# Kernel tuning notes

Hardware: AMD Instinct MI355X
Metric: run time of the kernel (lower is better)

The kernel has to match this reference:

```python
import jax, jax.numpy as jnp
import numpy as np


def setup_inputs() -> dict:
    key = jax.random.key(0)
    kq, kk, kv = jax.random.split(key, 3)
    B, H, S, D = 2, 16, 2048, 64
    query = jax.random.normal(kq, (B, H, S, D), dtype=jnp.float32)
    k = jax.random.normal(kk, (B, H, S, D), dtype=jnp.float32)
    value = jax.random.normal(kv, (B, H, S, D), dtype=jnp.float32)
    attn_mask = jnp.zeros((B, H, S, S), dtype=jnp.float32)
    return {"query": query, "key": k, "value": value, "attn_mask": attn_mask}


def reference(query, key, value, attn_mask):
    # scores: [B, H, Lq, Lk]
    dk = jnp.asarray(query.shape[-1], query.dtype)
    scores = jnp.einsum("bhqd,bhkd->bhqk", query, key) / jnp.sqrt(dk)
    scores = scores + attn_mask
    attention = jax.nn.softmax(scores, axis=-1)
    # dropout is identity at inference (training=False)
    context = jnp.einsum("bhqk,bhkd->bhqd", attention, value)
    return (context, attention)
```

## Files before the change

kernel.cpp:

```cpp
#include <hip/hip_runtime.h>
#include <stdint.h>


#if defined(__has_builtin)
#if __has_builtin(__builtin_amdgcn_exp2f)
#define EXP2(x) __builtin_amdgcn_exp2f(x)
#else
#define EXP2(x) exp2f(x)
#endif
#else
#define EXP2(x) exp2f(x)
#endif

typedef _Float16 half8 __attribute__((ext_vector_type(8)));
typedef _Float16 half2v __attribute__((ext_vector_type(2)));
typedef float f32x4 __attribute__((ext_vector_type(4)));

static constexpr int S = 2048;
static constexpr int D = 64;
static constexpr int BH = 32;
static constexpr int QT = 16;
static constexpr float LOG2E = 1.4426950408889634f;
static constexpr float SCL2E = 0.125f * LOG2E;

__device__ __forceinline__ half8 cvt8(float4 a, float4 b) {
  half8 r;
  r[0] = (_Float16)a.x; r[1] = (_Float16)a.y; r[2] = (_Float16)a.z; r[3] = (_Float16)a.w;
  r[4] = (_Float16)b.x; r[5] = (_Float16)b.y; r[6] = (_Float16)b.z; r[7] = (_Float16)b.w;
  return r;
}

__device__ __forceinline__ unsigned pack2(float a, float b) {
  half2v h; h[0] = (_Float16)a; h[1] = (_Float16)b;
  return __builtin_bit_cast(unsigned, h);
}

__device__ __forceinline__ float2 unpack2(unsigned u) {
  half2v h = __builtin_bit_cast(half2v, u);
  return make_float2((float)h[0], (float)h[1]);
}

__global__ __launch_bounds__(256, 3)
void sdpa_kernel(const float* __restrict__ Qg, const float* __restrict__ Kg,
                 const float* __restrict__ Vg, const float* __restrict__ Mg,
                 float* __restrict__ Cg, float* __restrict__ Ag) {
  const int bh = blockIdx.x & (BH - 1);
  const int qt = blockIdx.x >> 5;

  const int tid  = threadIdx.x;
  const int w    = tid >> 6;
  const int lane = tid & 63;
  const int quad = lane >> 4;
  const int l16  = lane & 15;

  const int q0 = qt * QT;
  const float* Qb = Qg + (size_t)bh * S * D;
  const float* Kb = Kg + (size_t)bh * S * D;
  const float* Vb = Vg + (size_t)bh * S * D;
  const float* Mb = Mg + (size_t)bh * S * S;
  float* Ab = Ag + (size_t)bh * S * S;
  float* Cb = Cg + (size_t)bh * S * D;

  __shared__ float partial[4][16];
  __shared__ float invsum[16];
  __shared__ _Float16 pbuf[4][16 * 72];
  __shared__ float ctxbuf[4][16 * 68];

  half8 a0, a1;
  {
    const float* qp = Qb + (size_t)(q0 + l16) * D + quad * 8;
    float4 x0 = *(const float4*)(qp);
    float4 x1 = *(const float4*)(qp + 4);
    float4 x2 = *(const float4*)(qp + 32);
    float4 x3 = *(const float4*)(qp + 36);
    a0 = cvt8(x0, x1);
    a1 = cvt8(x2, x3);
  }

  const int c0 = w * 512;
  float rs0 = 0.f, rs1 = 0.f, rs2 = 0.f, rs3 = 0.f;
  uint2 strip[32];

#pragma unroll
  for (int t = 0; t < 32; ++t) {
    const int col = c0 + t * 16;
    const int n   = col + l16;
    const float* kp = Kb + (size_t)n * D + quad * 8;
    float4 k0 = *(const float4*)(kp);
    float4 k1 = *(const float4*)(kp + 4);
    float4 k2 = *(const float4*)(kp + 32);
    float4 k3 = *(const float4*)(kp + 36);
    const float* mp = Mb + (size_t)(q0 + quad * 4) * S + n;
    float m0 = mp[0];
    float m1 = mp[S];
    float m2 = mp[2 * S];
    float m3 = mp[3 * S];

    half8 b0 = cvt8(k0, k1);
    half8 b1 = cvt8(k2, k3);
    f32x4 acc = {0.f, 0.f, 0.f, 0.f};
    acc = __builtin_amdgcn_mfma_f32_16x16x32_f16(a0, b0, acc, 0, 0, 0);
    acc = __builtin_amdgcn_mfma_f32_16x16x32_f16(a1, b1, acc, 0, 0, 0);

    float p0 = EXP2(fmaf(acc[0], SCL2E, m0 * LOG2E));
    float p1 = EXP2(fmaf(acc[1], SCL2E, m1 * LOG2E));
    float p2 = EXP2(fmaf(acc[2], SCL2E, m2 * LOG2E));
    float p3 = EXP2(fmaf(acc[3], SCL2E, m3 * LOG2E));
    rs0 += p0; rs1 += p1; rs2 += p2; rs3 += p3;
    strip[t].x = pack2(p0, p1);
    strip[t].y = pack2(p2, p3);
  }

#pragma unroll
  for (int off = 8; off >= 1; off >>= 1) {
    rs0 += __shfl_xor(rs0, off, 64);
    rs1 += __shfl_xor(rs1, off, 64);
    rs2 += __shfl_xor(rs2, off, 64);
    rs3 += __shfl_xor(rs3, off, 64);
  }
  if (l16 == 0) {
    partial[w][quad * 4 + 0] = rs0;
    partial[w][quad * 4 + 1] = rs1;
    partial[w][quad * 4 + 2] = rs2;
    partial[w][quad * 4 + 3] = rs3;
  }
  __syncthreads();
  if (tid < 16) {
    float s = partial[0][tid] + partial[1][tid] + partial[2][tid] + partial[3][tid];
    invsum[tid] = 1.0f / s;
  }
  __syncthreads();
  const float inv0 = invsum[quad * 4 + 0];
  const float inv1 = invsum[quad * 4 + 1];
  const float inv2 = invsum[quad * 4 + 2];
  const float inv3 = invsum[quad * 4 + 3];

#pragma unroll
  for (int t = 0; t < 32; ++t) {
    const int col = c0 + t * 16 + l16;
    float2 p01 = unpack2(strip[t].x);
    float2 p23 = unpack2(strip[t].y);
    float* ap = Ab + (size_t)(q0 + quad * 4) * S + col;
    ap[0]     = p01.x * inv0;
    ap[S]     = p01.y * inv1;
    ap[2 * S] = p23.x * inv2;
    ap[3 * S] = p23.y * inv3;
  }

  f32x4 ctx[4] = {{0.f,0.f,0.f,0.f},{0.f,0.f,0.f,0.f},{0.f,0.f,0.f,0.f},{0.f,0.f,0.f,0.f}};
  _Float16* pb = &pbuf[w][0];
#pragma unroll
  for (int c = 0; c < 8; ++c) {
    __syncthreads();
#pragma unroll
    for (int tt = 0; tt < 4; ++tt) {
      const int t = c * 4 + tt;
      half2v h01 = __builtin_bit_cast(half2v, strip[t].x);
      half2v h23 = __builtin_bit_cast(half2v, strip[t].y);
      const int colc = tt * 16 + l16;
      pb[(quad * 4 + 0) * 72 + colc] = h01[0];
      pb[(quad * 4 + 1) * 72 + colc] = h01[1];
      pb[(quad * 4 + 2) * 72 + colc] = h23[0];
      pb[(quad * 4 + 3) * 72 + colc] = h23[1];
    }
    __syncthreads();
    const int ks0 = c0 + c * 64;
#pragma unroll
    for (int kk = 0; kk < 2; ++kk) {
      half8 af = *(const half8*)(pb + l16 * 72 + kk * 32 + quad * 8);
      const float* vp = Vb + (size_t)(ks0 + kk * 32 + quad * 8) * D + l16;
#pragma unroll
      for (int nt = 0; nt < 4; ++nt) {
        const float* vq = vp + nt * 16;
        half8 bf;
#pragma unroll
        for (int j = 0; j < 8; ++j) bf[j] = (_Float16)vq[(size_t)j * D];
        ctx[nt] = __builtin_amdgcn_mfma_f32_16x16x32_f16(af, bf, ctx[nt], 0, 0, 0);
      }
    }
  }

#pragma unroll
  for (int nt = 0; nt < 4; ++nt) {
    float* cb = &ctxbuf[w][0];
    const int colc = nt * 16 + l16;
    cb[(quad * 4 + 0) * 68 + colc] = ctx[nt][0] * inv0;
    cb[(quad * 4 + 1) * 68 + colc] = ctx[nt][1] * inv1;
    cb[(quad * 4 + 2) * 68 + colc] = ctx[nt][2] * inv2;
    cb[(quad * 4 + 3) * 68 + colc] = ctx[nt][3] * inv3;
  }
  __syncthreads();
#pragma unroll
  for (int i = 0; i < 4; ++i) {
    const int e = tid + 256 * i;
    const int m = e >> 6;
    const int n = e & 63;
    float v = ctxbuf[0][m * 68 + n] + ctxbuf[1][m * 68 + n] +
              ctxbuf[2][m * 68 + n] + ctxbuf[3][m * 68 + n];
    Cb[(size_t)(q0 + m) * D + n] = v;
  }
}

extern "C" void kernel_launch(void* const* d_in, const int* in_sizes, int n_in,
                              void* d_out, int out_size, void* d_ws, size_t ws_size,
                              hipStream_t stream) {
  (void)in_sizes; (void)n_in; (void)d_ws; (void)ws_size; (void)out_size;
  const float* Q = (const float*)d_in[0];
  const float* K = (const float*)d_in[1];
  const float* V = (const float*)d_in[2];
  const float* M = (const float*)d_in[3];
  float* ctx  = (float*)d_out;
  float* attn = (float*)d_out + (size_t)2 * 16 * 2048 * 64;
  sdpa_kernel<<<dim3(BH * (S / QT)), dim3(256), 0, stream>>>(Q, K, V, M, ctx, attn);
}
```

Measured before the change: 1.231 ms.

## Prefetch mask/K loads, fuse coalesced attention stores into PV loop, share LDS

Software-pipelines the QK stage. Mask values are prefetched four tiles ahead with nontemporal loads, and the K tile is prefetched one step ahead. The separate attention-store pass is removed. The normalized probabilities are now written from the per-wave LDS tile inside the PV loop as full 64-lane contiguous row segments, using nontemporal stores. The P and context LDS buffers are merged into one union, the per-chunk block barriers are dropped because each wave uses its own buffer, and launch bounds are raised to 4 blocks per CU. This trades more register pressure and reliance on in-wave LDS ordering for better memory-level parallelism and store coalescing.

```diff
diff --git a/kernel.cpp b/kernel.cpp
--- a/kernel.cpp
+++ b/kernel.cpp
@@ -35,12 +35,7 @@
   return __builtin_bit_cast(unsigned, h);
 }
 
-__device__ __forceinline__ float2 unpack2(unsigned u) {
-  half2v h = __builtin_bit_cast(half2v, u);
-  return make_float2((float)h[0], (float)h[1]);
-}
-
-__global__ __launch_bounds__(256, 3)
+__global__ __launch_bounds__(256, 4)
 void sdpa_kernel(const float* __restrict__ Qg, const float* __restrict__ Kg,
                  const float* __restrict__ Vg, const float* __restrict__ Mg,
                  float* __restrict__ Cg, float* __restrict__ Ag) {
@@ -63,8 +58,7 @@
 
   __shared__ float partial[4][16];
   __shared__ float invsum[16];
-  __shared__ _Float16 pbuf[4][16 * 72];
-  __shared__ float ctxbuf[4][16 * 68];
+  __shared__ __align__(16) unsigned char uni[4][4352];
 
   half8 a0, a1;
   {
@@ -81,31 +75,51 @@
   float rs0 = 0.f, rs1 = 0.f, rs2 = 0.f, rs3 = 0.f;
   uint2 strip[32];
 
+  const float* mr0 = Mb + (size_t)(q0 + quad * 4) * S + c0 + l16;
+  const float* mr1 = mr0 + S;
+  const float* mr2 = mr0 + 2 * S;
+  const float* mr3 = mr0 + 3 * S;
+  const float* kb0 = Kb + (size_t)(c0 + l16) * D + quad * 8;
+
+  float4 mq[4];
+#pragma unroll
+  for (int i = 0; i < 4; ++i) {
+    mq[i].x = __builtin_nontemporal_load(mr0 + i * 16);
+    mq[i].y = __builtin_nontemporal_load(mr1 + i * 16);
+    mq[i].z = __builtin_nontemporal_load(mr2 + i * 16);
+    mq[i].w = __builtin_nontemporal_load(mr3 + i * 16);
+  }
+  float4 k0 = *(const float4*)(kb0);
+  float4 k1 = *(const float4*)(kb0 + 4);
+  float4 k2 = *(const float4*)(kb0 + 32);
+  float4 k3 = *(const float4*)(kb0 + 36);
+
 #pragma unroll
   for (int t = 0; t < 32; ++t) {
-    const int col = c0 + t * 16;
-    const int n   = col + l16;
-    const float* kp = Kb + (size_t)n * D + quad * 8;
-    float4 k0 = *(const float4*)(kp);
-    float4 k1 = *(const float4*)(kp + 4);
-    float4 k2 = *(const float4*)(kp + 32);
-    float4 k3 = *(const float4*)(kp + 36);
-    const float* mp = Mb + (size_t)(q0 + quad * 4) * S + n;
-    float m0 = mp[0];
-    float m1 = mp[S];
-    float m2 = mp[2 * S];
-    float m3 = mp[3 * S];
-
+    const float4 mm = mq[t & 3];
+    if (t + 4 < 32) {
+      mq[t & 3].x = __builtin_nontemporal_load(mr0 + (t + 4) * 16);
+      mq[t & 3].y = __builtin_nontemporal_load(mr1 + (t + 4) * 16);
+      mq[t & 3].z = __builtin_nontemporal_load(mr2 + (t + 4) * 16);
+      mq[t & 3].w = __builtin_nontemporal_load(mr3 + (t + 4) * 16);
+    }
     half8 b0 = cvt8(k0, k1);
     half8 b1 = cvt8(k2, k3);
+    if (t + 1 < 32) {
+      const float* kp = kb0 + (size_t)(t + 1) * 16 * D;
+      k0 = *(const float4*)(kp);
+      k1 = *(const float4*)(kp + 4);
+      k2 = *(const float4*)(kp + 32);
+      k3 = *(const float4*)(kp + 36);
+    }
     f32x4 acc = {0.f, 0.f, 0.f, 0.f};
     acc = __builtin_amdgcn_mfma_f32_16x16x32_f16(a0, b0, acc, 0, 0, 0);
     acc = __builtin_amdgcn_mfma_f32_16x16x32_f16(a1, b1, acc, 0, 0, 0);
 
-    float p0 = EXP2(fmaf(acc[0], SCL2E, m0 * LOG2E));
-    float p1 = EXP2(fmaf(acc[1], SCL2E, m1 * LOG2E));
-    float p2 = EXP2(fmaf(acc[2], SCL2E, m2 * LOG2E));
-    float p3 = EXP2(fmaf(acc[3], SCL2E, m3 * LOG2E));
+    float p0 = EXP2(fmaf(acc[0], SCL2E, mm.x * LOG2E));
+    float p1 = EXP2(fmaf(acc[1], SCL2E, mm.y * LOG2E));
+    float p2 = EXP2(fmaf(acc[2], SCL2E, mm.z * LOG2E));
+    float p3 = EXP2(fmaf(acc[3], SCL2E, mm.w * LOG2E));
     rs0 += p0; rs1 += p1; rs2 += p2; rs3 += p3;
     strip[t].x = pack2(p0, p1);
     strip[t].y = pack2(p2, p3);
@@ -135,23 +149,10 @@
   const float inv2 = invsum[quad * 4 + 2];
   const float inv3 = invsum[quad * 4 + 3];
 
-#pragma unroll
-  for (int t = 0; t < 32; ++t) {
-    const int col = c0 + t * 16 + l16;
-    float2 p01 = unpack2(strip[t].x);
-    float2 p23 = unpack2(strip[t].y);
-    float* ap = Ab + (size_t)(q0 + quad * 4) * S + col;
-    ap[0]     = p01.x * inv0;
-    ap[S]     = p01.y * inv1;
-    ap[2 * S] = p23.x * inv2;
-    ap[3 * S] = p23.y * inv3;
-  }
-
   f32x4 ctx[4] = {{0.f,0.f,0.f,0.f},{0.f,0.f,0.f,0.f},{0.f,0.f,0.f,0.f},{0.f,0.f,0.f,0.f}};
-  _Float16* pb = &pbuf[w][0];
+  _Float16* pb = (_Float16*)(&uni[w][0]);
 #pragma unroll
   for (int c = 0; c < 8; ++c) {
-    __syncthreads();
 #pragma unroll
     for (int tt = 0; tt < 4; ++tt) {
       const int t = c * 4 + tt;
@@ -163,7 +164,6 @@
       pb[(quad * 4 + 2) * 72 + colc] = h23[0];
       pb[(quad * 4 + 3) * 72 + colc] = h23[1];
     }
-    __syncthreads();
     const int ks0 = c0 + c * 64;
 #pragma unroll
     for (int kk = 0; kk < 2; ++kk) {
@@ -178,11 +178,18 @@
         ctx[nt] = __builtin_amdgcn_mfma_f32_16x16x32_f16(af, bf, ctx[nt], 0, 0, 0);
       }
     }
-  }
-
+    float* arow = Ab + (size_t)q0 * S + ks0 + lane;
+#pragma unroll
+    for (int r = 0; r < 16; ++r) {
+      const float iv = invsum[r];
+      float v = (float)pb[r * 72 + lane] * iv;
+      __builtin_nontemporal_store(v, arow + (size_t)r * S);
+    }
+  }
+
+  float* cb = (float*)(&uni[w][0]);
 #pragma unroll
   for (int nt = 0; nt < 4; ++nt) {
-    float* cb = &ctxbuf[w][0];
     const int colc = nt * 16 + l16;
     cb[(quad * 4 + 0) * 68 + colc] = ctx[nt][0] * inv0;
     cb[(quad * 4 + 1) * 68 + colc] = ctx[nt][1] * inv1;
@@ -190,14 +197,20 @@
     cb[(quad * 4 + 3) * 68 + colc] = ctx[nt][3] * inv3;
   }
   __syncthreads();
-#pragma unroll
-  for (int i = 0; i < 4; ++i) {
-    const int e = tid + 256 * i;
-    const int m = e >> 6;
-    const int n = e & 63;
-    float v = ctxbuf[0][m * 68 + n] + ctxbuf[1][m * 68 + n] +
-              ctxbuf[2][m * 68 + n] + ctxbuf[3][m * 68 + n];
-    Cb[(size_t)(q0 + m) * D + n] = v;
+  {
+    const float* cb0 = (const float*)(&uni[0][0]);
+    const float* cb1 = (const float*)(&uni[1][0]);
+    const float* cb2 = (const float*)(&uni[2][0]);
+    const float* cb3 = (const float*)(&uni[3][0]);
+#pragma unroll
+    for (int i = 0; i < 4; ++i) {
+      const int e = tid + 256 * i;
+      const int m = e >> 6;
+      const int n = e & 63;
+      float v = cb0[m * 68 + n] + cb1[m * 68 + n] +
+                cb2[m * 68 + n] + cb3[m * 68 + n];
+      Cb[(size_t)(q0 + m) * D + n] = v;
+    }
   }
 }
 
```

Result: slower. 1.718 ms (+39.5%).
